# Optimization experiments

Hardware: AMD Instinct MI355X
Metric: run time of the kernel (lower is better)

The kernel has to match this reference:

```python
import jax, jax.numpy as jnp
from jax import lax
import numpy as np

NPOINT, K, EPS = 2048, 16, 1e-5


def fps(xyz, npoint):
    # Farthest point sampling. Deterministic start index 0 (torch uses randint).
    B, N, _ = xyz.shape
    def step(carry, _):
        distance, far = carry
        centroid = jnp.take_along_axis(xyz, far[:, None, None], axis=1)  # [B,1,3]
        d = jnp.sum((xyz - centroid) ** 2, axis=-1)                      # [B,N]
        distance = jnp.minimum(distance, d)
        return (distance, jnp.argmax(distance, axis=-1)), far
    init = (jnp.full((B, N), 1e10, dtype=xyz.dtype), jnp.zeros((B,), jnp.int32))
    _, cent = lax.scan(step, init, None, length=npoint)  # [npoint, B]
    return jnp.transpose(cent)  # [B, npoint]


def gather(points, idx):
    # points [B,N,C], idx [B,...] -> [B,...,C]
    return jax.vmap(lambda p, i: p[i])(points, idx)


def bn_relu(x, gamma, beta):
    # x [B,S,K,C]; BatchNorm2d training-mode stats over (B,S,K) per channel
    mu = jnp.mean(x, axis=(0, 1, 2), keepdims=True)
    var = jnp.var(x, axis=(0, 1, 2), keepdims=True)
    return jax.nn.relu((x - mu) * lax.rsqrt(var + EPS) * gamma + beta)


def setup_inputs() -> dict:
    key = jax.random.key(0)
    ks = jax.random.split(key, 8)
    B, N, C_in, C_out = 4, 8192, 64, 128
    return {
        'xyz': jax.random.normal(ks[0], (B, N, 3), jnp.float32),
        'feat': jax.random.normal(ks[1], (B, N, C_in), jnp.float32),
        'W1': jax.random.normal(ks[2], (C_in + 3, C_out), jnp.float32) * 0.05,
        'g1': jnp.ones((C_out,), jnp.float32),
        'b1': jnp.zeros((C_out,), jnp.float32),
        'W2': jax.random.normal(ks[3], (C_out, C_out), jnp.float32) * 0.05,
        'g2': jnp.ones((C_out,), jnp.float32),
        'b2': jnp.zeros((C_out,), jnp.float32),
    }


def reference(xyz, feat, W1, g1, b1, W2, g2, b2):
    fps_idx = fps(xyz, NPOINT)
    new_xyz = gather(xyz, fps_idx)                              # [B,S,3]
    # squared distances [B,S,N] via ||a||^2 + ||b||^2 - 2 a.b (avoids [B,S,N,3])
    d = (jnp.sum(new_xyz ** 2, -1)[:, :, None]
         + jnp.sum(xyz ** 2, -1)[:, None, :]
         - 2.0 * jnp.einsum('bsc,bnc->bsn', new_xyz, xyz))
    _, idx = lax.top_k(-d, K)                                   # [B,S,K] smallest dists
    g_xyz = gather(xyz, idx)                                    # [B,S,K,3]
    g_feat = gather(feat, idx)                                  # [B,S,K,C]
    x = jnp.concatenate([g_feat, g_xyz - new_xyz[:, :, None]], axis=-1)
    x = bn_relu(jnp.einsum('bskc,co->bsko', x, W1), g1, b1)     # 1x1 conv == matmul
    x = bn_relu(jnp.einsum('bskc,co->bsko', x, W2), g2, b2)
    new_feat = jnp.max(x, axis=2)                               # max over K -> [B,S,Cout]
    return new_xyz, new_feat
```

## Files before the change

kernel.cpp:

```cpp
#include <hip/hip_runtime.h>
#include <hip/hip_bf16.h>

#define N_PTS 8192
#define N_SAMP 2048
#define KNN_K 16
#define NBATCH 4
#define BN_M (NBATCH * N_SAMP * KNN_K)
#define NROWS (N_SAMP * NBATCH * KNN_K)

typedef float f32x2 __attribute__((ext_vector_type(2)));

__device__ __forceinline__ f32x2 pk_sub(f32x2 a, f32x2 b) {
  f32x2 d;
  asm("v_pk_add_f32 %0, %1, %2 neg_lo:[0,1] neg_hi:[0,1]" : "=v"(d) : "v"(a), "v"(b));
  return d;
}
__device__ __forceinline__ f32x2 pk_mul(f32x2 a, f32x2 b) {
  f32x2 d; asm("v_pk_mul_f32 %0, %1, %2" : "=v"(d) : "v"(a), "v"(b)); return d;
}
__device__ __forceinline__ f32x2 pk_add2(f32x2 a, f32x2 b) {
  f32x2 d; asm("v_pk_add_f32 %0, %1, %2" : "=v"(d) : "v"(a), "v"(b)); return d;
}
__device__ __forceinline__ float max3f(float a, float b, float c) {
  float d; asm("v_max3_f32 %0, %1, %2, %3" : "=v"(d) : "v"(a), "v"(b), "v"(c)); return d;
}

template <int CTRL, int RM>
__device__ __forceinline__ unsigned umax_dpp(unsigned v) {
  unsigned o = (unsigned)__builtin_amdgcn_update_dpp((int)v, (int)v, CTRL, RM, 0xF, false);
  return (o > v) ? o : v;
}
template <int CTRL, int RM>
__device__ __forceinline__ unsigned umin_dpp(unsigned v) {
  unsigned o = (unsigned)__builtin_amdgcn_update_dpp((int)v, (int)v, CTRL, RM, 0xF, false);
  return (o < v) ? o : v;
}
template <int CTRL, int RM>
__device__ __forceinline__ unsigned long long kmax_dpp(unsigned long long k) {
  int lo = (int)(unsigned)k, hi = (int)(unsigned)(k >> 32);
  int lo2 = __builtin_amdgcn_update_dpp(lo, lo, CTRL, RM, 0xF, false);
  int hi2 = __builtin_amdgcn_update_dpp(hi, hi, CTRL, RM, 0xF, false);
  unsigned long long o = ((unsigned long long)(unsigned)hi2 << 32) | (unsigned)lo2;
  return (o > k) ? o : k;
}

__global__ __launch_bounds__(512) void fps_kernel(const float* __restrict__ xyz,
                                                  int* __restrict__ fps_idx,
                                                  float* __restrict__ new_xyz) {
#pragma clang fp contract(off)
  __shared__ __align__(16) float xyzw[N_PTS * 4];
  __shared__ int samp[N_SAMP];
  __shared__ unsigned long long redbuf[2][8];
  const int b = blockIdx.x;
  const int tid = threadIdx.x;
  const int lane = tid & 63;
  const int wid = tid >> 6;
  const float* base = xyz + (size_t)b * N_PTS * 3;
  for (int i = tid; i < N_PTS * 3; i += 512) {
    float v = base[i];
    int p = i / 3, c = i - p * 3;
    xyzw[p * 4 + c] = v;
  }
  for (int i = tid; i < N_PTS; i += 512) xyzw[i * 4 + 3] = 0.f;
  if (tid == 0) samp[0] = 0;
  __syncthreads();

  f32x2 px[8], py[8], pz[8], dmin[8];
#pragma unroll
  for (int j = 0; j < 8; ++j) {
    int p0 = (2 * j) * 512 + tid, p1 = p0 + 512;
    const float4 a = *reinterpret_cast<const float4*>(&xyzw[p0 * 4]);
    const float4 c = *reinterpret_cast<const float4*>(&xyzw[p1 * 4]);
    px[j] = f32x2{a.x, c.x};
    py[j] = f32x2{a.y, c.y};
    pz[j] = f32x2{a.z, c.z};
    dmin[j] = f32x2{1e10f, 1e10f};
  }
  unsigned cur = 0;
  for (int it = 1; it < N_SAMP; ++it) {
    const float4 c4 = *reinterpret_cast<const float4*>(&xyzw[cur * 4]);
    f32x2 cX = {c4.x, c4.x}, cY = {c4.y, c4.y}, cZ = {c4.z, c4.z};
#pragma unroll
    for (int j = 0; j < 8; ++j) {
      f32x2 dx = pk_sub(px[j], cX);
      f32x2 dy = pk_sub(py[j], cY);
      f32x2 dz = pk_sub(pz[j], cZ);
      f32x2 xx = pk_mul(dx, dx);
      f32x2 yy = pk_mul(dy, dy);
      f32x2 zz = pk_mul(dz, dz);
      f32x2 d = pk_add2(pk_add2(xx, yy), zz);
      dmin[j] = __builtin_elementwise_min(dmin[j], d);
    }
    float t0 = max3f(dmin[0].x, dmin[0].y, dmin[1].x);
    float t1 = max3f(dmin[1].y, dmin[2].x, dmin[2].y);
    float t2 = max3f(dmin[3].x, dmin[3].y, dmin[4].x);
    float t3 = max3f(dmin[4].y, dmin[5].x, dmin[5].y);
    float t4 = max3f(dmin[6].x, dmin[6].y, dmin[7].x);
    float u0 = max3f(t0, t1, t2);
    float u1 = max3f(t3, t4, dmin[7].y);
    const unsigned bd = __float_as_uint(fmaxf(u0, u1));
    unsigned r = bd;
    r = umax_dpp<0xB1, 0xF>(r);
    r = umax_dpp<0x4E, 0xF>(r);
    r = umax_dpp<0x124, 0xF>(r);
    r = umax_dpp<0x128, 0xF>(r);
    r = umax_dpp<0x142, 0xA>(r);
    r = umax_dpp<0x143, 0xC>(r);
    const unsigned g_wave = (unsigned)__builtin_amdgcn_readlane((int)r, 63);
    unsigned cand = 0xFFFFFFFFu;
#pragma unroll
    for (int j = 7; j >= 0; --j) {
      cand = (__float_as_uint(dmin[j].y) == g_wave) ? (unsigned)((2 * j + 1) * 512 + tid) : cand;
      cand = (__float_as_uint(dmin[j].x) == g_wave) ? (unsigned)((2 * j) * 512 + tid) : cand;
    }
    cand = umin_dpp<0xB1, 0xF>(cand);
    cand = umin_dpp<0x4E, 0xF>(cand);
    cand = umin_dpp<0x124, 0xF>(cand);
    cand = umin_dpp<0x128, 0xF>(cand);
    cand = umin_dpp<0x142, 0xA>(cand);
    cand = umin_dpp<0x143, 0xC>(cand);
    const unsigned c_wave = (unsigned)__builtin_amdgcn_readlane((int)cand, 63);
    if (lane == 0)
      redbuf[it & 1][wid] = ((unsigned long long)g_wave << 32) | (unsigned)(0x3FFF - c_wave);
    __syncthreads();
    unsigned long long k2 = redbuf[it & 1][lane & 7];
    k2 = kmax_dpp<0xB1, 0xF>(k2);
    k2 = kmax_dpp<0x4E, 0xF>(k2);
    k2 = kmax_dpp<0x124, 0xF>(k2);
    cur = 0x3FFFu - (unsigned)(k2 & 0xFFFFFFFFu);
    if (tid == 0) samp[it] = (int)cur;
  }
  __syncthreads();
  for (int s = tid; s < N_SAMP; s += 512) {
    int idx = samp[s];
    fps_idx[b * N_SAMP + s] = idx;
    size_t o = ((size_t)b * N_SAMP + s) * 3;
    new_xyz[o] = xyzw[idx * 4 + 0];
    new_xyz[o + 1] = xyzw[idx * 4 + 1];
    new_xyz[o + 2] = xyzw[idx * 4 + 2];
  }
}

__global__ __launch_bounds__(256) void knn_kernel(const float* __restrict__ xyz,
                                                  const float* __restrict__ new_xyz,
                                                  int* __restrict__ knn_idx) {
  const int wid = threadIdx.x >> 6, lane = threadIdx.x & 63;
  const int q = blockIdx.x * 4 + wid;
  const int b = q >> 11;
  const float* qp = new_xyz + (size_t)q * 3;
  float q0 = qp[0], q1 = qp[1], q2 = qp[2];
  float qn = __fadd_rn(__fadd_rn(__fmul_rn(q0, q0), __fmul_rn(q1, q1)), __fmul_rn(q2, q2));
  const float* pb = xyz + (size_t)b * N_PTS * 3;
  unsigned long long arr[16];
#pragma unroll
  for (int i = 0; i < 16; ++i) arr[i] = ~0ull;
  for (int p = lane; p < N_PTS; p += 64) {
    float p0 = pb[p * 3 + 0], p1 = pb[p * 3 + 1], p2 = pb[p * 3 + 2];
    float pn = __fadd_rn(__fadd_rn(__fmul_rn(p0, p0), __fmul_rn(p1, p1)), __fmul_rn(p2, p2));
    float dt = fmaf(q2, p2, fmaf(q1, p1, __fmul_rn(q0, p0)));
    float d = __fsub_rn(__fadd_rn(qn, pn), __fmul_rn(2.0f, dt));
    unsigned ub = __float_as_uint(d);
    ub ^= (unsigned)((int)ub >> 31) | 0x80000000u;
    unsigned long long key = ((unsigned long long)ub << 32) | (unsigned)p;
    if (key < arr[15]) {
      unsigned long long curk = key;
#pragma unroll
      for (int j = 0; j < 16; ++j) {
        unsigned long long lo = (curk < arr[j]) ? curk : arr[j];
        unsigned long long hi = (curk < arr[j]) ? arr[j] : curk;
        arr[j] = lo; curk = hi;
      }
    }
  }
  for (int r = 0; r < KNN_K; ++r) {
    unsigned long long m = arr[0];
#pragma unroll
    for (int o = 32; o > 0; o >>= 1) {
      unsigned long long other = __shfl_xor(m, o, 64);
      m = (other < m) ? other : m;
    }
    if (arr[0] == m) {
#pragma unroll
      for (int j = 0; j < 15; ++j) arr[j] = arr[j + 1];
      arr[15] = ~0ull;
    }
    if (lane == r) knn_idx[(size_t)q * KNN_K + r] = (int)(m & 0xFFFFFFFFu);
  }
}

__global__ __launch_bounds__(256) void gemm1_kernel(
    const float* __restrict__ xyz, const float* __restrict__ feat,
    const float* __restrict__ W1, const float* __restrict__ new_xyz,
    const int* __restrict__ knn_i, float* __restrict__ y1, float* __restrict__ stats1) {
  __shared__ __align__(16) float At[67 * 128];
  __shared__ __align__(16) float Wq[17 * 128];
  __shared__ float part[4 * 256];
  __shared__ int nb[128];
  const int t = threadIdx.x, blk = blockIdx.x;
  const int row0 = blk * 128;
  if (t < 128) nb[t] = knn_i[row0 + t];
  __syncthreads();
  {
    const int r = t >> 1, q = t & 1;
    const int rg = row0 + r, bs = rg >> 4, b = bs >> 11;
    const float* fr = feat + ((size_t)b * N_PTS + nb[r]) * 64 + q * 32;
#pragma unroll
    for (int i = 0; i < 8; ++i) {
      float4 v = *reinterpret_cast<const float4*>(fr + 4 * i);
      int c = q * 32 + 4 * i;
      At[(c + 0) * 128 + r] = v.x; At[(c + 1) * 128 + r] = v.y;
      At[(c + 2) * 128 + r] = v.z; At[(c + 3) * 128 + r] = v.w;
    }
    if (q == 0) {
      const float* pr = xyz + ((size_t)b * N_PTS + nb[r]) * 3;
      const float* qr = new_xyz + (size_t)bs * 3;
      At[64 * 128 + r] = pr[0] - qr[0];
      At[65 * 128 + r] = pr[1] - qr[1];
      At[66 * 128 + r] = pr[2] - qr[2];
    }
  }
  float acc[8][8];
#pragma unroll
  for (int i = 0; i < 8; ++i)
#pragma unroll
    for (int j = 0; j < 8; ++j) acc[i][j] = 0.f;
  const int ry = t >> 4, cx = t & 15;
  for (int kq = 0; kq < 4; ++kq) {
    const int kbase = kq * 17;
    const int nk = (67 - kbase) < 17 ? (67 - kbase) : 17;
    __syncthreads();
    for (int i = t; i < nk * 32; i += 256)
      reinterpret_cast<float4*>(Wq)[i] =
          reinterpret_cast<const float4*>(W1 + (size_t)kbase * 128)[i];
    __syncthreads();
    for (int kk = 0; kk < nk; ++kk) {
      const float4 a0 = *reinterpret_cast<const float4*>(&At[(kbase + kk) * 128 + ry * 8]);
      const float4 a1 = *reinterpret_cast<const float4*>(&At[(kbase + kk) * 128 + ry * 8 + 4]);
      const float4 w0 = *reinterpret_cast<const float4*>(&Wq[kk * 128 + cx * 8]);
      const float4 w1 = *reinterpret_cast<const float4*>(&Wq[kk * 128 + cx * 8 + 4]);
      const float a[8] = {a0.x, a0.y, a0.z, a0.w, a1.x, a1.y, a1.z, a1.w};
      const float w[8] = {w0.x, w0.y, w0.z, w0.w, w1.x, w1.y, w1.z, w1.w};
#pragma unroll
      for (int i = 0; i < 8; ++i)
#pragma unroll
        for (int j = 0; j < 8; ++j) acc[i][j] = fmaf(a[i], w[j], acc[i][j]);
    }
  }
#pragma unroll
  for (int i = 0; i < 8; ++i) {
    float4 v0 = {acc[i][0], acc[i][1], acc[i][2], acc[i][3]};
    float4 v1 = {acc[i][4], acc[i][5], acc[i][6], acc[i][7]};
    float* dst = y1 + ((size_t)row0 + ry * 8 + i) * 128 + cx * 8;
    *reinterpret_cast<float4*>(dst) = v0;
    *reinterpret_cast<float4*>(dst + 4) = v1;
  }
  float s8[8], q8[8];
#pragma unroll
  for (int j = 0; j < 8; ++j) {
    s8[j] = 0.f; q8[j] = 0.f;
#pragma unroll
    for (int i = 0; i < 8; ++i) { s8[j] += acc[i][j]; q8[j] += acc[i][j] * acc[i][j]; }
  }
#pragma unroll
  for (int j = 0; j < 8; ++j) {
    s8[j] += __shfl_xor(s8[j], 16, 64); q8[j] += __shfl_xor(q8[j], 16, 64);
    s8[j] += __shfl_xor(s8[j], 32, 64); q8[j] += __shfl_xor(q8[j], 32, 64);
  }
  const int w = t >> 6, lane = t & 63;
  if (lane < 16) {
#pragma unroll
    for (int j = 0; j < 8; ++j) {
      part[w * 256 + lane * 8 + j] = s8[j];
      part[w * 256 + 128 + lane * 8 + j] = q8[j];
    }
  }
  __syncthreads();
  {
    int ch = t & 127, which = t >> 7;
    float v = part[0 * 256 + which * 128 + ch] + part[1 * 256 + which * 128 + ch] +
              part[2 * 256 + which * 128 + ch] + part[3 * 256 + which * 128 + ch];
    atomicAdd(&stats1[which * 128 + ch], v);
  }
}

__global__ __launch_bounds__(256) void gemm2_kernel(
    const float* __restrict__ y1, const float* __restrict__ W2,
    const float* __restrict__ stats1, const float* __restrict__ g1v,
    const float* __restrict__ b1v, float* __restrict__ y2, float* __restrict__ stats2) {
  __shared__ __align__(16) float Ah[64 * 128];
  __shared__ __align__(16) float Wq[32 * 128];
  __shared__ float part[4 * 256];
  __shared__ float s1[128], h1[128];
  const int t = threadIdx.x, blk = blockIdx.x;
  const int row0 = blk * 128;
  const float inv_m = 1.0f / (float)BN_M;
  if (t < 128) {
    float m = stats1[t] * inv_m;
    float var = stats1[128 + t] * inv_m - m * m;
    float rs = rsqrtf(var + 1e-5f);
    float sc = rs * g1v[t];
    s1[t] = sc;
    h1[t] = b1v[t] - m * sc;
  }
  float acc[8][8];
#pragma unroll
  for (int i = 0; i < 8; ++i)
#pragma unroll
    for (int j = 0; j < 8; ++j) acc[i][j] = 0.f;
  const int ry = t >> 4, cx = t & 15;
  for (int kh = 0; kh < 2; ++kh) {
    __syncthreads();
    {
      const int r = t >> 1, q = t & 1;
      const float* src = y1 + ((size_t)row0 + r) * 128 + kh * 64 + q * 32;
#pragma unroll
      for (int i = 0; i < 8; ++i) {
        float4 v = *reinterpret_cast<const float4*>(src + 4 * i);
        int c = kh * 64 + q * 32 + 4 * i;
        int cl = c - kh * 64;
        Ah[(cl + 0) * 128 + r] = fmaxf(fmaf(v.x, s1[c + 0], h1[c + 0]), 0.f);
        Ah[(cl + 1) * 128 + r] = fmaxf(fmaf(v.y, s1[c + 1], h1[c + 1]), 0.f);
        Ah[(cl + 2) * 128 + r] = fmaxf(fmaf(v.z, s1[c + 2], h1[c + 2]), 0.f);
        Ah[(cl + 3) * 128 + r] = fmaxf(fmaf(v.w, s1[c + 3], h1[c + 3]), 0.f);
      }
    }
    for (int kq = 0; kq < 2; ++kq) {
      __syncthreads();
      const int kbase = kh * 64 + kq * 32;
      for (int i = t; i < 32 * 32; i += 256)
        reinterpret_cast<float4*>(Wq)[i] =
            reinterpret_cast<const float4*>(W2 + (size_t)kbase * 128)[i];
      __syncthreads();
      for (int kk = 0; kk < 32; ++kk) {
        const int kl = kq * 32 + kk;
        const float4 a0 = *reinterpret_cast<const float4*>(&Ah[kl * 128 + ry * 8]);
        const float4 a1 = *reinterpret_cast<const float4*>(&Ah[kl * 128 + ry * 8 + 4]);
        const float4 w0 = *reinterpret_cast<const float4*>(&Wq[kk * 128 + cx * 8]);
        const float4 w1 = *reinterpret_cast<const float4*>(&Wq[kk * 128 + cx * 8 + 4]);
        const float a[8] = {a0.x, a0.y, a0.z, a0.w, a1.x, a1.y, a1.z, a1.w};
        const float w[8] = {w0.x, w0.y, w0.z, w0.w, w1.x, w1.y, w1.z, w1.w};
#pragma unroll
        for (int i = 0; i < 8; ++i)
#pragma unroll
          for (int j = 0; j < 8; ++j) acc[i][j] = fmaf(a[i], w[j], acc[i][j]);
      }
    }
  }
#pragma unroll
  for (int i = 0; i < 8; ++i) {
    float4 v0 = {acc[i][0], acc[i][1], acc[i][2], acc[i][3]};
    float4 v1 = {acc[i][4], acc[i][5], acc[i][6], acc[i][7]};
    float* dst = y2 + ((size_t)row0 + ry * 8 + i) * 128 + cx * 8;
    *reinterpret_cast<float4*>(dst) = v0;
    *reinterpret_cast<float4*>(dst + 4) = v1;
  }
  float s8[8], q8[8];
#pragma unroll
  for (int j = 0; j < 8; ++j) {
    s8[j] = 0.f; q8[j] = 0.f;
#pragma unroll
    for (int i = 0; i < 8; ++i) { s8[j] += acc[i][j]; q8[j] += acc[i][j] * acc[i][j]; }
  }
#pragma unroll
  for (int j = 0; j < 8; ++j) {
    s8[j] += __shfl_xor(s8[j], 16, 64); q8[j] += __shfl_xor(q8[j], 16, 64);
    s8[j] += __shfl_xor(s8[j], 32, 64); q8[j] += __shfl_xor(q8[j], 32, 64);
  }
  const int w = t >> 6, lane = t & 63;
  if (lane < 16) {
#pragma unroll
    for (int j = 0; j < 8; ++j) {
      part[w * 256 + lane * 8 + j] = s8[j];
      part[w * 256 + 128 + lane * 8 + j] = q8[j];
    }
  }
  __syncthreads();
  {
    int ch = t & 127, which = t >> 7;
    float v = part[0 * 256 + which * 128 + ch] + part[1 * 256 + which * 128 + ch] +
              part[2 * 256 + which * 128 + ch] + part[3 * 256 + which * 128 + ch];
    atomicAdd(&stats2[which * 128 + ch], v);
  }
}

__global__ __launch_bounds__(256) void pool_kernel(
    const float* __restrict__ y2, const float* __restrict__ stats2,
    const float* __restrict__ g2v, const float* __restrict__ b2v,
    float* __restrict__ out_feat) {
  __shared__ float s2[128], h2[128];
  __shared__ float part[4 * 128];
  const int t = threadIdx.x, blk = blockIdx.x;
  const float inv_m = 1.0f / (float)BN_M;
  if (t < 128) {
    float m = stats2[t] * inv_m;
    float var = stats2[128 + t] * inv_m - m * m;
    float rs = rsqrtf(var + 1e-5f);
    float sc = rs * g2v[t];
    s2[t] = sc;
    h2[t] = b2v[t] - m * sc;
  }
  __syncthreads();
  const int c4 = (t & 31) * 4, rg = t >> 5;
  const int lane = t & 63, w = t >> 6;
  for (int s = 0; s < 8; ++s) {
    const int bs = blk * 8 + s;
    float4 m4 = {-1e30f, -1e30f, -1e30f, -1e30f};
#pragma unroll
    for (int rr = 0; rr < 2; ++rr) {
      const int r = bs * 16 + rg * 2 + rr;
      float4 v = *reinterpret_cast<const float4*>(y2 + (size_t)r * 128 + c4);
      float4 z = {fmaxf(fmaf(v.x, s2[c4 + 0], h2[c4 + 0]), 0.f),
                  fmaxf(fmaf(v.y, s2[c4 + 1], h2[c4 + 1]), 0.f),
                  fmaxf(fmaf(v.z, s2[c4 + 2], h2[c4 + 2]), 0.f),
                  fmaxf(fmaf(v.w, s2[c4 + 3], h2[c4 + 3]), 0.f)};
      m4.x = fmaxf(m4.x, z.x); m4.y = fmaxf(m4.y, z.y);
      m4.z = fmaxf(m4.z, z.z); m4.w = fmaxf(m4.w, z.w);
    }
    m4.x = fmaxf(m4.x, __shfl_xor(m4.x, 32, 64));
    m4.y = fmaxf(m4.y, __shfl_xor(m4.y, 32, 64));
    m4.z = fmaxf(m4.z, __shfl_xor(m4.z, 32, 64));
    m4.w = fmaxf(m4.w, __shfl_xor(m4.w, 32, 64));
    if (lane < 32) {
      part[w * 128 + c4 + 0] = m4.x; part[w * 128 + c4 + 1] = m4.y;
      part[w * 128 + c4 + 2] = m4.z; part[w * 128 + c4 + 3] = m4.w;
    }
    __syncthreads();
    if (t < 128) {
      float mm = fmaxf(fmaxf(part[t], part[128 + t]), fmaxf(part[256 + t], part[384 + t]));
      out_feat[(size_t)bs * 128 + t] = mm;
    }
    __syncthreads();
  }
}

extern "C" void kernel_launch(void* const* d_in, const int* in_sizes, int n_in,
                              void* d_out, int out_size, void* d_ws, size_t ws_size,
                              hipStream_t stream) {
  const float* xyz  = (const float*)d_in[0];
  const float* feat = (const float*)d_in[1];
  const float* W1   = (const float*)d_in[2];
  const float* g1   = (const float*)d_in[3];
  const float* b1   = (const float*)d_in[4];
  const float* W2   = (const float*)d_in[5];
  const float* g2   = (const float*)d_in[6];
  const float* b2   = (const float*)d_in[7];
  float* out = (float*)d_out;
  float* new_xyz = out;
  float* out_feat = out + NBATCH * N_SAMP * 3;

  int* fps_i = (int*)d_ws;
  int* knn_i = fps_i + NBATCH * N_SAMP;
  float* stats1 = (float*)(knn_i + NROWS);
  float* stats2 = stats1 + 256;
  float* y1 = stats2 + 256;
  float* y2 = y1 + (size_t)NROWS * 128;

  hipMemsetAsync(stats1, 0, 512 * sizeof(float), stream);
  hipLaunchKernelGGL(fps_kernel, dim3(NBATCH), dim3(512), 0, stream, xyz, fps_i, new_xyz);
  hipLaunchKernelGGL(knn_kernel, dim3((NBATCH * N_SAMP) / 4), dim3(256), 0, stream,
                     xyz, new_xyz, knn_i);
  hipLaunchKernelGGL(gemm1_kernel, dim3(NROWS / 128), dim3(256), 0, stream,
                     xyz, feat, W1, new_xyz, knn_i, y1, stats1);
  hipLaunchKernelGGL(gemm2_kernel, dim3(NROWS / 128), dim3(256), 0, stream,
                     y1, W2, stats1, g1, b1, y2, stats2);
  hipLaunchKernelGGL(pool_kernel, dim3(NBATCH * N_SAMP / 8), dim3(256), 0, stream,
                     y2, stats2, g2, b2, out_feat);
}
```

Before: 2.446 ms.

## Widen FPS block to 1024 threads and split argmax into two barrier phases

The FPS kernel now runs 1024 threads per batch, so each thread holds 8 points instead of 16. The per-iteration reduction is reordered: waves first reduce only the max distance and agree on the global max through shared memory. Only the waves that hold that max then search for the lowest matching index and publish it with an LDS atomicMin. The inline packed-math asm is replaced with plain vector expressions. This shortens each thread's serial work in the 2047-step loop but adds a second block barrier per iteration and an atomic step.

```diff
diff --git a/kernel.cpp b/kernel.cpp
--- a/kernel.cpp
+++ b/kernel.cpp
@@ -10,21 +10,6 @@
 
 typedef float f32x2 __attribute__((ext_vector_type(2)));
 
-__device__ __forceinline__ f32x2 pk_sub(f32x2 a, f32x2 b) {
-  f32x2 d;
-  asm("v_pk_add_f32 %0, %1, %2 neg_lo:[0,1] neg_hi:[0,1]" : "=v"(d) : "v"(a), "v"(b));
-  return d;
-}
-__device__ __forceinline__ f32x2 pk_mul(f32x2 a, f32x2 b) {
-  f32x2 d; asm("v_pk_mul_f32 %0, %1, %2" : "=v"(d) : "v"(a), "v"(b)); return d;
-}
-__device__ __forceinline__ f32x2 pk_add2(f32x2 a, f32x2 b) {
-  f32x2 d; asm("v_pk_add_f32 %0, %1, %2" : "=v"(d) : "v"(a), "v"(b)); return d;
-}
-__device__ __forceinline__ float max3f(float a, float b, float c) {
-  float d; asm("v_max3_f32 %0, %1, %2, %3" : "=v"(d) : "v"(a), "v"(b), "v"(c)); return d;
-}
-
 template <int CTRL, int RM>
 __device__ __forceinline__ unsigned umax_dpp(unsigned v) {
   unsigned o = (unsigned)__builtin_amdgcn_update_dpp((int)v, (int)v, CTRL, RM, 0xF, false);
@@ -35,40 +20,33 @@
   unsigned o = (unsigned)__builtin_amdgcn_update_dpp((int)v, (int)v, CTRL, RM, 0xF, false);
   return (o < v) ? o : v;
 }
-template <int CTRL, int RM>
-__device__ __forceinline__ unsigned long long kmax_dpp(unsigned long long k) {
-  int lo = (int)(unsigned)k, hi = (int)(unsigned)(k >> 32);
-  int lo2 = __builtin_amdgcn_update_dpp(lo, lo, CTRL, RM, 0xF, false);
-  int hi2 = __builtin_amdgcn_update_dpp(hi, hi, CTRL, RM, 0xF, false);
-  unsigned long long o = ((unsigned long long)(unsigned)hi2 << 32) | (unsigned)lo2;
-  return (o > k) ? o : k;
-}
-
-__global__ __launch_bounds__(512) void fps_kernel(const float* __restrict__ xyz,
-                                                  int* __restrict__ fps_idx,
-                                                  float* __restrict__ new_xyz) {
+
+__global__ __launch_bounds__(1024) void fps_kernel(const float* __restrict__ xyz,
+                                                   int* __restrict__ fps_idx,
+                                                   float* __restrict__ new_xyz) {
 #pragma clang fp contract(off)
   __shared__ __align__(16) float xyzw[N_PTS * 4];
   __shared__ int samp[N_SAMP];
-  __shared__ unsigned long long redbuf[2][8];
+  __shared__ unsigned redbuf[2][16];
+  __shared__ unsigned winmin[2];
   const int b = blockIdx.x;
   const int tid = threadIdx.x;
   const int lane = tid & 63;
   const int wid = tid >> 6;
   const float* base = xyz + (size_t)b * N_PTS * 3;
-  for (int i = tid; i < N_PTS * 3; i += 512) {
+  for (int i = tid; i < N_PTS * 3; i += 1024) {
     float v = base[i];
     int p = i / 3, c = i - p * 3;
     xyzw[p * 4 + c] = v;
   }
-  for (int i = tid; i < N_PTS; i += 512) xyzw[i * 4 + 3] = 0.f;
-  if (tid == 0) samp[0] = 0;
-  __syncthreads();
-
-  f32x2 px[8], py[8], pz[8], dmin[8];
-#pragma unroll
-  for (int j = 0; j < 8; ++j) {
-    int p0 = (2 * j) * 512 + tid, p1 = p0 + 512;
+  for (int i = tid; i < N_PTS; i += 1024) xyzw[i * 4 + 3] = 0.f;
+  if (tid == 0) { samp[0] = 0; winmin[0] = 0u; winmin[1] = 0xFFFFFFFFu; }
+  __syncthreads();
+
+  f32x2 px[4], py[4], pz[4], dmin[4];
+#pragma unroll
+  for (int j = 0; j < 4; ++j) {
+    int p0 = (2 * j) * 1024 + tid, p1 = p0 + 1024;
     const float4 a = *reinterpret_cast<const float4*>(&xyzw[p0 * 4]);
     const float4 c = *reinterpret_cast<const float4*>(&xyzw[p1 * 4]);
     px[j] = f32x2{a.x, c.x};
@@ -78,27 +56,22 @@
   }
   unsigned cur = 0;
   for (int it = 1; it < N_SAMP; ++it) {
+    const int p = it & 1;
     const float4 c4 = *reinterpret_cast<const float4*>(&xyzw[cur * 4]);
     f32x2 cX = {c4.x, c4.x}, cY = {c4.y, c4.y}, cZ = {c4.z, c4.z};
 #pragma unroll
-    for (int j = 0; j < 8; ++j) {
-      f32x2 dx = pk_sub(px[j], cX);
-      f32x2 dy = pk_sub(py[j], cY);
-      f32x2 dz = pk_sub(pz[j], cZ);
-      f32x2 xx = pk_mul(dx, dx);
-      f32x2 yy = pk_mul(dy, dy);
-      f32x2 zz = pk_mul(dz, dz);
-      f32x2 d = pk_add2(pk_add2(xx, yy), zz);
+    for (int j = 0; j < 4; ++j) {
+      f32x2 dx = px[j] - cX;
+      f32x2 dy = py[j] - cY;
+      f32x2 dz = pz[j] - cZ;
+      f32x2 s01 = dx * dx + dy * dy;
+      f32x2 d = s01 + dz * dz;
       dmin[j] = __builtin_elementwise_min(dmin[j], d);
     }
-    float t0 = max3f(dmin[0].x, dmin[0].y, dmin[1].x);
-    float t1 = max3f(dmin[1].y, dmin[2].x, dmin[2].y);
-    float t2 = max3f(dmin[3].x, dmin[3].y, dmin[4].x);
-    float t3 = max3f(dmin[4].y, dmin[5].x, dmin[5].y);
-    float t4 = max3f(dmin[6].x, dmin[6].y, dmin[7].x);
-    float u0 = max3f(t0, t1, t2);
-    float u1 = max3f(t3, t4, dmin[7].y);
-    const unsigned bd = __float_as_uint(fmaxf(u0, u1));
+    f32x2 m0 = __builtin_elementwise_max(dmin[0], dmin[1]);
+    f32x2 m1 = __builtin_elementwise_max(dmin[2], dmin[3]);
+    f32x2 nn = __builtin_elementwise_max(m0, m1);
+    const unsigned bd = __float_as_uint(fmaxf(nn.x, nn.y));
     unsigned r = bd;
     r = umax_dpp<0xB1, 0xF>(r);
     r = umax_dpp<0x4E, 0xF>(r);
@@ -107,31 +80,35 @@
     r = umax_dpp<0x142, 0xA>(r);
     r = umax_dpp<0x143, 0xC>(r);
     const unsigned g_wave = (unsigned)__builtin_amdgcn_readlane((int)r, 63);
-    unsigned cand = 0xFFFFFFFFu;
-#pragma unroll
-    for (int j = 7; j >= 0; --j) {
-      cand = (__float_as_uint(dmin[j].y) == g_wave) ? (unsigned)((2 * j + 1) * 512 + tid) : cand;
-      cand = (__float_as_uint(dmin[j].x) == g_wave) ? (unsigned)((2 * j) * 512 + tid) : cand;
-    }
-    cand = umin_dpp<0xB1, 0xF>(cand);
-    cand = umin_dpp<0x4E, 0xF>(cand);
-    cand = umin_dpp<0x124, 0xF>(cand);
-    cand = umin_dpp<0x128, 0xF>(cand);
-    cand = umin_dpp<0x142, 0xA>(cand);
-    cand = umin_dpp<0x143, 0xC>(cand);
-    const unsigned c_wave = (unsigned)__builtin_amdgcn_readlane((int)cand, 63);
-    if (lane == 0)
-      redbuf[it & 1][wid] = ((unsigned long long)g_wave << 32) | (unsigned)(0x3FFF - c_wave);
-    __syncthreads();
-    unsigned long long k2 = redbuf[it & 1][lane & 7];
-    k2 = kmax_dpp<0xB1, 0xF>(k2);
-    k2 = kmax_dpp<0x4E, 0xF>(k2);
-    k2 = kmax_dpp<0x124, 0xF>(k2);
-    cur = 0x3FFFu - (unsigned)(k2 & 0xFFFFFFFFu);
-    if (tid == 0) samp[it] = (int)cur;
-  }
-  __syncthreads();
-  for (int s = tid; s < N_SAMP; s += 512) {
+    if (lane == 0) redbuf[p][wid] = g_wave;
+    __syncthreads();
+    unsigned g2 = redbuf[p][lane & 15];
+    g2 = umax_dpp<0xB1, 0xF>(g2);
+    g2 = umax_dpp<0x4E, 0xF>(g2);
+    g2 = umax_dpp<0x124, 0xF>(g2);
+    g2 = umax_dpp<0x128, 0xF>(g2);
+    if (g_wave == g2) {
+      unsigned cand = 0xFFFFFFFFu;
+#pragma unroll
+      for (int j = 3; j >= 0; --j) {
+        cand = (__float_as_uint(dmin[j].y) == g2) ? (unsigned)((2 * j + 1) * 1024 + tid) : cand;
+        cand = (__float_as_uint(dmin[j].x) == g2) ? (unsigned)((2 * j) * 1024 + tid) : cand;
+      }
+      cand = umin_dpp<0xB1, 0xF>(cand);
+      cand = umin_dpp<0x4E, 0xF>(cand);
+      cand = umin_dpp<0x124, 0xF>(cand);
+      cand = umin_dpp<0x128, 0xF>(cand);
+      cand = umin_dpp<0x142, 0xA>(cand);
+      cand = umin_dpp<0x143, 0xC>(cand);
+      const unsigned c_wave = (unsigned)__builtin_amdgcn_readlane((int)cand, 63);
+      if (lane == 0) atomicMin(&winmin[p], c_wave);
+    }
+    __syncthreads();
+    cur = winmin[p];
+    if (tid == 0) { samp[it] = (int)cur; winmin[p ^ 1] = 0xFFFFFFFFu; }
+  }
+  __syncthreads();
+  for (int s = tid; s < N_SAMP; s += 1024) {
     int idx = samp[s];
     fps_idx[b * N_SAMP + s] = idx;
     size_t o = ((size_t)b * N_SAMP + s) * 3;
@@ -456,7 +433,7 @@
   float* y2 = y1 + (size_t)NROWS * 128;
 
   hipMemsetAsync(stats1, 0, 512 * sizeof(float), stream);
-  hipLaunchKernelGGL(fps_kernel, dim3(NBATCH), dim3(512), 0, stream, xyz, fps_i, new_xyz);
+  hipLaunchKernelGGL(fps_kernel, dim3(NBATCH), dim3(1024), 0, stream, xyz, fps_i, new_xyz);
   hipLaunchKernelGGL(knn_kernel, dim3((NBATCH * N_SAMP) / 4), dim3(256), 0, stream,
                      xyz, new_xyz, knn_i);
   hipLaunchKernelGGL(gemm1_kernel, dim3(NROWS / 128), dim3(256), 0, stream,
```

Measured after the change: 2.323 ms. -5.0%, faster.
